# Kernel optimization log

Measured on AMD Instinct MI355X. Metric: run time of the kernel, lower is better.

Reference implementation:

```python
import jax, jax.numpy as jnp
import numpy as np

N = 100000   # nodes
E = 800000   # directed edges (symmetrized to 2E in forward)
D0 = 128     # input feature dim (dim0)
H = 128      # hidden = h_dim * args.d = 64 * 2
L = 4        # num_layers
G = 64       # num graphs for global_mean_pool
BN_EPS = 1e-5
LN_EPS = 1e-5


def setup_inputs() -> dict:
    key = jax.random.key(0)
    ks = jax.random.split(key, 12)
    s = 1.0 / np.sqrt(H)
    x = jax.random.normal(ks[0], (N, D0), dtype=jnp.float32)
    row = jax.random.randint(ks[1], (E,), 0, N, dtype=jnp.int32)
    off = jax.random.randint(ks[2], (E,), 1, N, dtype=jnp.int32)
    col = (row + off) % N  # guarantees row != col (no self loops)
    edge_index = jnp.stack([row, col])
    batch = jnp.sort(jax.random.randint(ks[3], (N,), 0, G, dtype=jnp.int32))
    return {
        "x": x,
        "W0": jax.random.normal(ks[4], (D0, H), dtype=jnp.float32) * s,
        "b0": jnp.zeros((H,), jnp.float32),
        "eps_l": jnp.zeros((L,), jnp.float32),        # GIN eps per layer
        "W1": jax.random.normal(ks[5], (L, H, H), dtype=jnp.float32) * s,
        "b1": jnp.zeros((L, H), jnp.float32),
        "bn_g": jnp.ones((L, H), jnp.float32),
        "bn_b": jnp.zeros((L, H), jnp.float32),
        "W2": jax.random.normal(ks[6], (L, H, H), dtype=jnp.float32) * s,
        "b2": jnp.zeros((L, H), jnp.float32),
        "ln_g": jnp.ones((L, H), jnp.float32),
        "ln_b": jnp.zeros((L, H), jnp.float32),
        "edge_index": edge_index,
        "batch": batch,
    }


def reference(x, W0, b0, eps_l, W1, b1, bn_g, bn_b, W2, b2, ln_g, ln_b, edge_index, batch):
    n = x.shape[0]
    h = x @ W0 + b0  # layer0 encode -> [N, H]
    # FNSD: symmetrize edges (cat with flip) and drop self loops
    ei = jnp.concatenate([edge_index, edge_index[::-1]], axis=1)
    row, col = ei[0], ei[1]
    w = (row != col).astype(h.dtype)  # self-loop removal as zero edge weight
    for i in range(L):
        # GINConv: scatter-add of neighbor features
        agg = jax.ops.segment_sum(w[:, None] * h[col], row, num_segments=n)
        u = (1.0 + eps_l[i]) * h + agg
        # mlp: Linear -> BatchNorm1d (training-mode batch stats) -> ReLU -> Linear
        z = u @ W1[i] + b1[i]
        m = jnp.mean(z, axis=0)
        v = jnp.var(z, axis=0)
        z = (z - m) * jax.lax.rsqrt(v + BN_EPS) * bn_g[i] + bn_b[i]
        z = jax.nn.relu(z)
        z = z @ W2[i] + b2[i]
        z = jax.nn.relu(z)          # use_activation
        h = h + z                    # use_residual
        mu = jnp.mean(h, axis=-1, keepdims=True)   # LayerNorm
        var = jnp.var(h, axis=-1, keepdims=True)
        h = (h - mu) * jax.lax.rsqrt(var + LN_EPS) * ln_g[i] + ln_b[i]
    # global_mean_pool over graph ids
    cnt = jax.ops.segment_sum(jnp.ones((n,), h.dtype), batch, num_segments=G)
    sums = jax.ops.segment_sum(h, batch, num_segments=G)
    return sums / jnp.maximum(cnt, 1.0)[:, None]
```

## Files before the change

kernel.cpp:

```cpp
#include <hip/hip_runtime.h>

#define NN 100000
#define EE 800000
#define HH 128
#define LL 4
#define GG 64
#define BN_EPS 1e-5f
#define LN_EPS 1e-5f
#define POOL_CHUNK 64
#define NBUK ((NN + 255) >> 8)
#define CAP 8192
#define BCHUNK 8192
#define UPITCH 136

typedef __attribute__((ext_vector_type(8))) short short8;
typedef __attribute__((ext_vector_type(4))) float f32x4;

__device__ inline unsigned short bf16_rne(float f) {
    unsigned u = __float_as_uint(f);
    return (unsigned short)((u + 0x7FFF + ((u >> 16) & 1)) >> 16);
}
__device__ inline float bf16_to_f32(unsigned short h) {
    return __uint_as_float((unsigned)h << 16);
}


__global__ void setup_kernel(const float* __restrict__ W0, const float* __restrict__ W1,
                             const float* __restrict__ W2, short* __restrict__ wt_hi,
                             int* __restrict__ bcur, float* __restrict__ colsum,
                             float* __restrict__ psum, float* __restrict__ pcnt) {
    int i = blockIdx.x * 256 + threadIdx.x;
    if (i < NBUK) bcur[i] = i * CAP;
    if (i < LL * HH * 2) colsum[i] = 0.f;
    if (i < GG * HH) psum[i] = 0.f;
    if (i < GG) pcnt[i] = 0.f;
    if (i < 9 * HH * HH) {
        int mat = i >> 14, rem = i & 16383;
        int n = rem >> 7, k = rem & 127;
        const float* src = (mat == 0) ? W0 : ((mat <= 4) ? W1 + (size_t)(mat - 1) * HH * HH
                                                         : W2 + (size_t)(mat - 5) * HH * HH);
        float v = src[(size_t)k * HH + n];
        int off = (mat << 14) + (((k >> 3) * 8 + (n >> 4)) << 7) + ((n & 15) << 3) + (k & 7);
        wt_hi[off] = (short)bf16_rne(v);
    }
}


__global__ __launch_bounds__(256) void bucket_scatter(const int* __restrict__ ei, int* __restrict__ bcur,
                                                      int* __restrict__ pairs) {
    __shared__ int h[NBUK];
    __shared__ int curb[NBUK];
    int tid = threadIdx.x;
    for (int i = tid; i < NBUK; i += 256) h[i] = 0;
    __syncthreads();
    int base = blockIdx.x * BCHUNK;
#pragma unroll 4
    for (int k = 0; k < BCHUNK / 256; k++) {
        int e = base + k * 256 + tid;
        if (e < 2 * EE) {
            int r = ei[e];
            int c = (e < EE) ? ei[e + EE] : ei[e - EE];
            if (r != c) atomicAdd(&h[r >> 8], 1);
        }
    }
    __syncthreads();
    for (int i = tid; i < NBUK; i += 256) {
        int n = h[i];
        curb[i] = n ? atomicAdd(&bcur[i], n) : 0;
    }
    __syncthreads();
#pragma unroll 4
    for (int k = 0; k < BCHUNK / 256; k++) {
        int e = base + k * 256 + tid;
        if (e < 2 * EE) {
            int r = ei[e];
            int c = (e < EE) ? ei[e + EE] : ei[e - EE];
            if (r != c) {
                int p = atomicAdd(&curb[r >> 8], 1);
                pairs[p] = ((r & 255) << 17) | c;
            }
        }
    }
}

__global__ __launch_bounds__(256) void bucket_build(const int* __restrict__ pairs, const int* __restrict__ bcur,
                                                    int* __restrict__ rp, int* __restrict__ re,
                                                    int* __restrict__ colidx) {
    __shared__ int hist[256], off[256], lcol[CAP];
    int b = blockIdx.x, tid = threadIdx.x;
    int s = b * CAP;
    int size = bcur[b] - s;
    hist[tid] = 0;
    __syncthreads();
    for (int i = tid; i < size; i += 256) atomicAdd(&hist[pairs[s + i] >> 17], 1);
    __syncthreads();
    off[tid] = hist[tid];
    __syncthreads();
    for (int o = 1; o < 256; o <<= 1) {
        int x = (tid >= o) ? off[tid - o] : 0;
        __syncthreads();
        off[tid] += x;
        __syncthreads();
    }
    int excl = (tid > 0) ? off[tid - 1] : 0;
    int r = (b << 8) + tid;
    if (r < NN) { rp[r] = s + excl; re[r] = s + off[tid]; }
    hist[tid] = excl;
    __syncthreads();
    for (int i = tid; i < size; i += 256) {
        int u = pairs[s + i];
        int p = atomicAdd(&hist[u >> 17], 1);
        lcol[p] = u & 0x1FFFF;
    }
    __syncthreads();
    for (int i = tid; i < size; i += 256) colidx[s + i] = lcol[i];
}


__global__ __launch_bounds__(256, 6) void fused_g1(
    const uint2* __restrict__ hbf2,
    const int* __restrict__ rp, const int* __restrict__ re,
    const int* __restrict__ colidx,
    const float* __restrict__ eps_l, int layer,
    const short* __restrict__ wt,
    const float* __restrict__ bias,
    unsigned short* __restrict__ z1_out,
    float* __restrict__ colsum, float* __restrict__ colsq)
{
    __shared__ __align__(16) unsigned short uls[64 * UPITCH];
    __shared__ float stats[2 * HH];
    int tid = threadIdx.x;
    int wave = tid >> 6, lane = tid & 63;
    int half = lane >> 5, sub = lane & 31;
    int lrow = lane & 15, kgrp = lane >> 4;
    int r0 = blockIdx.x * 64;
    stats[tid] = 0.f;
    float eps1 = 1.0f + eps_l[layer];

    int hw = wave * 2 + half;
    for (int rl = 0; rl < 8; rl++) {
        int row = hw * 8 + rl;
        int r = r0 + row;
        float a0 = 0.f, a1 = 0.f, a2 = 0.f, a3 = 0.f;
        if (r < NN) {
            uint2 sv = hbf2[(size_t)r * 32 + sub];
            a0 = bf16_to_f32((unsigned short)(sv.x & 0xFFFF)) * eps1;
            a1 = bf16_to_f32((unsigned short)(sv.x >> 16)) * eps1;
            a2 = bf16_to_f32((unsigned short)(sv.y & 0xFFFF)) * eps1;
            a3 = bf16_to_f32((unsigned short)(sv.y >> 16)) * eps1;
            int base = rp[r];
            int n = re[r] - base;
            for (int i = 0; i < n; i += 8) {
                uint2 v[8];
                int c[8];
#pragma unroll
                for (int j = 0; j < 8; j++) c[j] = (i + j < n) ? colidx[base + i + j] : -1;
#pragma unroll
                for (int j = 0; j < 8; j++)
                    v[j] = (c[j] >= 0) ? hbf2[(size_t)c[j] * 32 + sub] : make_uint2(0u, 0u);
#pragma unroll
                for (int j = 0; j < 8; j++) {
                    a0 += bf16_to_f32((unsigned short)(v[j].x & 0xFFFF));
                    a1 += bf16_to_f32((unsigned short)(v[j].x >> 16));
                    a2 += bf16_to_f32((unsigned short)(v[j].y & 0xFFFF));
                    a3 += bf16_to_f32((unsigned short)(v[j].y >> 16));
                }
            }
        }
        uint2 o;
        o.x = (unsigned)bf16_rne(a0) | ((unsigned)bf16_rne(a1) << 16);
        o.y = (unsigned)bf16_rne(a2) | ((unsigned)bf16_rne(a3) << 16);
        *(uint2*)&uls[row * UPITCH + sub * 4] = o;
    }
    __syncthreads();

    short8 az[4];
#pragma unroll
    for (int ks = 0; ks < 4; ks++)
        az[ks] = *(const short8*)&uls[(wave * 16 + lrow) * UPITCH + ks * 32 + kgrp * 8];
    __syncthreads();

    f32x4 acc[8];
#pragma unroll
    for (int c = 0; c < 8; c++) acc[c] = (f32x4){0.f, 0.f, 0.f, 0.f};
#pragma unroll
    for (int ks = 0; ks < 4; ks++) {
        int fb = (ks * 4 + kgrp) * 8;
#pragma unroll
        for (int c = 0; c < 8; c++) {
            short8 whi = *(const short8*)(wt + (size_t)((fb + c) << 7) + (lrow << 3));
            acc[c] = __builtin_amdgcn_mfma_f32_16x16x32_bf16(az[ks], whi, acc[c], 0, 0, 0);
        }
    }

    float bv[8];
#pragma unroll
    for (int c = 0; c < 8; c++) bv[c] = bias[c * 16 + lrow];
    int lrb = wave * 16 + kgrp * 4;
    float ps[8], pq[8];
#pragma unroll
    for (int c = 0; c < 8; c++) { ps[c] = 0.f; pq[c] = 0.f; }
#pragma unroll
    for (int c = 0; c < 8; c++)
#pragma unroll
        for (int reg = 0; reg < 4; reg++) {
            float z = acc[c][reg] + bv[c];
            uls[(lrb + reg) * UPITCH + c * 16 + lrow] = bf16_rne(z);
            if (r0 + lrb + reg < NN) { ps[c] += z; pq[c] += z * z; }
        }
#pragma unroll
    for (int c = 0; c < 8; c++) {
        ps[c] += __shfl_xor(ps[c], 16); pq[c] += __shfl_xor(pq[c], 16);
        ps[c] += __shfl_xor(ps[c], 32); pq[c] += __shfl_xor(pq[c], 32);
    }
    if (kgrp == 0) {
#pragma unroll
        for (int c = 0; c < 8; c++) {
            atomicAdd(&stats[c * 16 + lrow], ps[c]);
            atomicAdd(&stats[HH + c * 16 + lrow], pq[c]);
        }
    }
    __syncthreads();
#pragma unroll
    for (int i = 0; i < 4; i++) {
        int idx = tid + i * 256;
        int row = idx >> 4;
        int r = r0 + row;
        if (r < NN)
            *(uint4*)(z1_out + (size_t)r * HH + (idx & 15) * 8) =
                *(const uint4*)&uls[row * UPITCH + (idx & 15) * 8];
    }
    if (tid < HH) {
        atomicAdd(&colsum[tid], stats[tid]);
        atomicAdd(&colsq[tid], stats[HH + tid]);
    }
}


template<int MODE>
__global__ __launch_bounds__(256, 4) void gemm_v9(
    const void* __restrict__ Ain,
    const short* __restrict__ wt_hi,
    const float* __restrict__ bias,
    float* __restrict__ colsum, float* __restrict__ colsq,
    const float* __restrict__ bng, const float* __restrict__ bnb,
    const float* __restrict__ lng, const float* __restrict__ lnb,
    unsigned short* __restrict__ hbf)
{
    __shared__ short wh[HH * HH];
    __shared__ float stats[2 * HH];
    int tid = threadIdx.x;
    int wave = tid >> 6, lane = tid & 63;
    int lrow = lane & 15, kgrp = lane >> 4;
    int r0 = blockIdx.x * 64;
    int arow = r0 + wave * 16 + lrow;

    {
        const short8* src = (const short8*)wt_hi;
        short8* dst = (short8*)wh;
#pragma unroll
        for (int i = 0; i < 8; i++) dst[tid + i * 256] = src[tid + i * 256];
    }
    if (MODE == 2 && tid < HH) {
        float m = colsum[tid] * (1.f / NN);
        float v = colsq[tid] * (1.f / NN) - m * m;
        float a = bng[tid] * rsqrtf(v + BN_EPS);
        stats[tid] = a;
        stats[HH + tid] = bnb[tid] - m * a;
    }

    float4 a0[4], a1[4];
    short8 az[4];
    if (MODE == 2) {
        const unsigned short* Az = (const unsigned short*)Ain;
        if (arow < NN) {
#pragma unroll
            for (int ks = 0; ks < 4; ks++)
                az[ks] = *(const short8*)(Az + (size_t)arow * HH + ks * 32 + kgrp * 8);
        } else {
#pragma unroll
            for (int ks = 0; ks < 4; ks++) az[ks] = (short8){0,0,0,0,0,0,0,0};
        }
    } else {
        const float* Af = (const float*)Ain;
        if (arow < NN) {
#pragma unroll
            for (int ks = 0; ks < 4; ks++) {
                int kb = ks * 32 + kgrp * 8;
                a0[ks] = *(const float4*)(Af + (size_t)arow * HH + kb);
                a1[ks] = *(const float4*)(Af + (size_t)arow * HH + kb + 4);
            }
        } else {
#pragma unroll
            for (int ks = 0; ks < 4; ks++) {
                a0[ks] = make_float4(0.f, 0.f, 0.f, 0.f);
                a1[ks] = a0[ks];
            }
        }
    }
    __syncthreads();

    f32x4 acc[8];
#pragma unroll
    for (int c = 0; c < 8; c++) acc[c] = (f32x4){0.f, 0.f, 0.f, 0.f};

#pragma unroll
    for (int ks = 0; ks < 4; ks++) {
        int fb = (ks * 4 + kgrp) * 8;
        int kb = ks * 32 + kgrp * 8;
        float av[8];
        if (MODE == 2) {
#pragma unroll
            for (int j = 0; j < 8; j++) {
                float zb = bf16_to_f32((unsigned short)az[ks][j]);
                av[j] = fmaxf(fmaf(zb, stats[kb + j], stats[HH + kb + j]), 0.f);
            }
        } else {
            av[0] = a0[ks].x; av[1] = a0[ks].y; av[2] = a0[ks].z; av[3] = a0[ks].w;
            av[4] = a1[ks].x; av[5] = a1[ks].y; av[6] = a1[ks].z; av[7] = a1[ks].w;
        }
        short8 ahi, alo;
#pragma unroll
        for (int j = 0; j < 8; j++) {
            unsigned short hb = bf16_rne(av[j]);
            ahi[j] = (short)hb;
            alo[j] = (short)bf16_rne(av[j] - bf16_to_f32(hb));
        }
#pragma unroll
        for (int c = 0; c < 8; c++) {
            short8 whi = *(const short8*)(wh + ((fb + c) << 7) + (lrow << 3));
            acc[c] = __builtin_amdgcn_mfma_f32_16x16x32_bf16(ahi, whi, acc[c], 0, 0, 0);
            acc[c] = __builtin_amdgcn_mfma_f32_16x16x32_bf16(alo, whi, acc[c], 0, 0, 0);
        }
    }

    float bv[8];
#pragma unroll
    for (int c = 0; c < 8; c++) bv[c] = bias[c * 16 + lrow];
    int lrb = wave * 16 + kgrp * 4;
    unsigned short* hst = (unsigned short*)wh;

    if (MODE == 0) {
        __syncthreads();
#pragma unroll
        for (int c = 0; c < 8; c++)
#pragma unroll
            for (int reg = 0; reg < 4; reg++)
                hst[(lrb + reg) * HH + c * 16 + lrow] = bf16_rne(acc[c][reg] + bv[c]);
        __syncthreads();
#pragma unroll
        for (int i = 0; i < 4; i++) {
            int idx = tid + i * 256;
            int r = r0 + (idx >> 4);
            if (r < NN)
                *(uint4*)(hbf + (size_t)r * HH + (idx & 15) * 8) = ((const uint4*)wh)[idx];
        }
    } else {
        float lg[8], lb[8];
#pragma unroll
        for (int c = 0; c < 8; c++) {
            lg[c] = lng[c * 16 + lrow];
            lb[c] = lnb[c * 16 + lrow];
        }
        __syncthreads();
#pragma unroll
        for (int i = 0; i < 4; i++) {
            int idx = tid + i * 256;
            int r = r0 + (idx >> 4);
            uint4 v = make_uint4(0, 0, 0, 0);
            if (r < NN) v = *(const uint4*)(hbf + (size_t)r * HH + (idx & 15) * 8);
            ((uint4*)wh)[idx] = v;
        }
        __syncthreads();
#pragma unroll
        for (int reg = 0; reg < 4; reg++) {
            int r = r0 + lrb + reg;
            if (r < NN) {
                float tv[8];
                float s = 0.f, q = 0.f;
#pragma unroll
                for (int c = 0; c < 8; c++) {
                    float hold = bf16_to_f32(hst[(lrb + reg) * HH + c * 16 + lrow]);
                    tv[c] = hold + fmaxf(acc[c][reg] + bv[c], 0.f);
                    s += tv[c]; q += tv[c] * tv[c];
                }
#pragma unroll
                for (int m = 1; m < 16; m <<= 1) {
                    s += __shfl_xor(s, m);
                    q += __shfl_xor(q, m);
                }
                float mu = s * (1.f / 128.f);
                float var = q * (1.f / 128.f) - mu * mu;
                float rs = rsqrtf(var + LN_EPS);
#pragma unroll
                for (int c = 0; c < 8; c++)
                    hst[(lrb + reg) * HH + c * 16 + lrow] =
                        bf16_rne((tv[c] - mu) * rs * lg[c] + lb[c]);
            }
        }
        __syncthreads();
#pragma unroll
        for (int i = 0; i < 4; i++) {
            int idx = tid + i * 256;
            int r = r0 + (idx >> 4);
            if (r < NN)
                *(uint4*)(hbf + (size_t)r * HH + (idx & 15) * 8) = ((const uint4*)wh)[idx];
        }
    }
}


__global__ void pool_kernel(const unsigned short* __restrict__ h, const int* __restrict__ batch,
                            float* __restrict__ psum, float* __restrict__ pcnt)
{
    int t = threadIdx.x;
    int n0 = blockIdx.x * POOL_CHUNK;
    int n1 = n0 + POOL_CHUNK; if (n1 > NN) n1 = NN;
    if (n0 >= NN) return;
    float acc = 0.f;
    int cur = batch[n0];
    int cnt = 0;
    for (int n = n0; n < n1; n++) {
        int g = batch[n];
        if (g != cur) {
            atomicAdd(&psum[cur * HH + t], acc);
            if (t == 0) atomicAdd(&pcnt[cur], (float)cnt);
            acc = 0.f; cnt = 0; cur = g;
        }
        acc += bf16_to_f32(h[(size_t)n * HH + t]);
        cnt++;
    }
    atomicAdd(&psum[cur * HH + t], acc);
    if (t == 0) atomicAdd(&pcnt[cur], (float)cnt);
}

__global__ void pool_final(const float* __restrict__ psum, const float* __restrict__ pcnt,
                           float* __restrict__ out)
{
    int i = blockIdx.x * blockDim.x + threadIdx.x;
    if (i < GG * HH) {
        float c = pcnt[i >> 7];
        out[i] = psum[i] / fmaxf(c, 1.f);
    }
}


extern "C" void kernel_launch(void* const* d_in, const int* in_sizes, int n_in,
                              void* d_out, int out_size, void* d_ws, size_t ws_size,
                              hipStream_t stream)
{
    const float* x     = (const float*)d_in[0];
    const float* W0    = (const float*)d_in[1];
    const float* b0    = (const float*)d_in[2];
    const float* eps_l = (const float*)d_in[3];
    const float* W1    = (const float*)d_in[4];
    const float* b1    = (const float*)d_in[5];
    const float* bng   = (const float*)d_in[6];
    const float* bnb   = (const float*)d_in[7];
    const float* W2    = (const float*)d_in[8];
    const float* b2    = (const float*)d_in[9];
    const float* lng   = (const float*)d_in[10];
    const float* lnb   = (const float*)d_in[11];
    const int*   ei    = (const int*)d_in[12];
    const int*   batch = (const int*)d_in[13];
    float* out = (float*)d_out;

    char* ws = (char*)d_ws;
    size_t off = 0;
    auto alloc = [&](size_t bytes) -> void* {
        void* p = ws + off;
        off += (bytes + 255) & ~(size_t)255;
        return p;
    };
    unsigned short* hbf = (unsigned short*)alloc((size_t)NN * HH * 2);
    unsigned short* z1  = (unsigned short*)alloc((size_t)NN * HH * 2);
    int*   colidx = (int*)alloc((size_t)NBUK * CAP * 4 + 1024);
    int*   pairs  = (int*)alloc((size_t)NBUK * CAP * 4);
    int*   rp     = (int*)alloc((size_t)NN * 4);
    int*   re     = (int*)alloc((size_t)NN * 4);
    int*   bcur   = (int*)alloc((NBUK + 1) * 4);
    float* colsum = (float*)alloc((size_t)LL * HH * 2 * 4);
    float* psum   = (float*)alloc((size_t)GG * HH * 4);
    float* pcnt   = (float*)alloc(GG * 4);
    short* wt_hi  = (short*)alloc((size_t)9 * HH * HH * 2);

    setup_kernel<<<(9 * HH * HH + 255) / 256, 256, 0, stream>>>(W0, W1, W2, wt_hi, bcur,
                                                                colsum, psum, pcnt);

    bucket_scatter<<<(2 * EE + BCHUNK - 1) / BCHUNK, 256, 0, stream>>>(ei, bcur, pairs);
    bucket_build<<<NBUK, 256, 0, stream>>>(pairs, bcur, rp, re, colidx);

    int gb = (NN + 63) / 64;
    gemm_v9<0><<<gb, 256, 0, stream>>>(x, wt_hi, b0,
                                       nullptr, nullptr, nullptr, nullptr, nullptr, nullptr, hbf);

    for (int l = 0; l < LL; l++) {
        float* cs = colsum + (size_t)l * HH * 2;
        float* cq = cs + HH;
        fused_g1<<<gb, 256, 0, stream>>>((const uint2*)hbf, rp, re, colidx, eps_l, l,
                                         wt_hi + (size_t)(1 + l) * HH * HH, b1 + l * HH, z1,
                                         cs, cq);
        gemm_v9<2><<<gb, 256, 0, stream>>>(z1, wt_hi + (size_t)(5 + l) * HH * HH,
                                           b2 + l * HH,
                                           cs, cq, bng + l * HH, bnb + l * HH,
                                           lng + l * HH, lnb + l * HH, hbf);
    }

    pool_kernel<<<(NN + POOL_CHUNK - 1) / POOL_CHUNK, 128, 0, stream>>>(hbf, batch, psum, pcnt);
    pool_final<<<(GG * HH + 255) / 256, 256, 0, stream>>>(psum, pcnt, out);
}
```

Baseline: 675.0 us.

## Restructure GIN aggregation to 16-lane uint4 gathers with 32-row blocks

```diff
diff --git a/kernel.cpp b/kernel.cpp
--- a/kernel.cpp
+++ b/kernel.cpp
@@ -12,6 +12,7 @@
 #define CAP 8192
 #define BCHUNK 8192
 #define UPITCH 136
+#define BR 32
 
 typedef __attribute__((ext_vector_type(8))) short short8;
 typedef __attribute__((ext_vector_type(4))) float f32x4;
@@ -117,8 +118,8 @@
 }
 
 
-__global__ __launch_bounds__(256, 6) void fused_g1(
-    const uint2* __restrict__ hbf2,
+__global__ __launch_bounds__(256, 8) void fused_g1(
+    const uint4* __restrict__ hbf4,
     const int* __restrict__ rp, const int* __restrict__ re,
     const int* __restrict__ colidx,
     const float* __restrict__ eps_l, int layer,
@@ -127,102 +128,126 @@
     unsigned short* __restrict__ z1_out,
     float* __restrict__ colsum, float* __restrict__ colsq)
 {
-    __shared__ __align__(16) unsigned short uls[64 * UPITCH];
+    __shared__ __align__(16) unsigned short uls[BR * UPITCH];
     __shared__ float stats[2 * HH];
     int tid = threadIdx.x;
     int wave = tid >> 6, lane = tid & 63;
-    int half = lane >> 5, sub = lane & 31;
     int lrow = lane & 15, kgrp = lane >> 4;
-    int r0 = blockIdx.x * 64;
+    int sub = lrow;
+    int qw = wave * 4 + kgrp;
+    int r0 = blockIdx.x * BR;
     stats[tid] = 0.f;
     float eps1 = 1.0f + eps_l[layer];
 
-    int hw = wave * 2 + half;
-    for (int rl = 0; rl < 8; rl++) {
-        int row = hw * 8 + rl;
+    int base_[2], n_[2];
+#pragma unroll
+    for (int rl = 0; rl < 2; rl++) {
+        int r = r0 + qw * 2 + rl;
+        if (r < NN) { base_[rl] = rp[r]; n_[rl] = re[r] - base_[rl]; }
+        else        { base_[rl] = 0;     n_[rl] = 0; }
+    }
+    for (int rl = 0; rl < 2; rl++) {
+        int row = qw * 2 + rl;
         int r = r0 + row;
-        float a0 = 0.f, a1 = 0.f, a2 = 0.f, a3 = 0.f;
-        if (r < NN) {
-            uint2 sv = hbf2[(size_t)r * 32 + sub];
-            a0 = bf16_to_f32((unsigned short)(sv.x & 0xFFFF)) * eps1;
-            a1 = bf16_to_f32((unsigned short)(sv.x >> 16)) * eps1;
-            a2 = bf16_to_f32((unsigned short)(sv.y & 0xFFFF)) * eps1;
-            a3 = bf16_to_f32((unsigned short)(sv.y >> 16)) * eps1;
-            int base = rp[r];
-            int n = re[r] - base;
-            for (int i = 0; i < n; i += 8) {
-                uint2 v[8];
-                int c[8];
-#pragma unroll
-                for (int j = 0; j < 8; j++) c[j] = (i + j < n) ? colidx[base + i + j] : -1;
-#pragma unroll
-                for (int j = 0; j < 8; j++)
-                    v[j] = (c[j] >= 0) ? hbf2[(size_t)c[j] * 32 + sub] : make_uint2(0u, 0u);
-#pragma unroll
-                for (int j = 0; j < 8; j++) {
-                    a0 += bf16_to_f32((unsigned short)(v[j].x & 0xFFFF));
-                    a1 += bf16_to_f32((unsigned short)(v[j].x >> 16));
-                    a2 += bf16_to_f32((unsigned short)(v[j].y & 0xFFFF));
-                    a3 += bf16_to_f32((unsigned short)(v[j].y >> 16));
-                }
+        uint4 sv = make_uint4(0u, 0u, 0u, 0u);
+        if (r < NN) sv = hbf4[(size_t)r * 16 + sub];
+        int base = base_[rl], n = n_[rl];
+        float a[8];
+#pragma unroll
+        for (int j = 0; j < 8; j++) a[j] = 0.f;
+        for (int i = 0; i < n; i += 8) {
+            uint4 v[8];
+            int c[4];
+#pragma unroll
+            for (int j = 0; j < 4; j++) c[j] = (i + j < n) ? colidx[base + i + j] : -1;
+#pragma unroll
+            for (int j = 0; j < 4; j++)
+                v[j] = (c[j] >= 0) ? hbf4[(size_t)c[j] * 16 + sub] : make_uint4(0u, 0u, 0u, 0u);
+#pragma unroll
+            for (int j = 0; j < 4; j++) c[j] = (i + 4 + j < n) ? colidx[base + i + 4 + j] : -1;
+#pragma unroll
+            for (int j = 0; j < 4; j++)
+                v[4 + j] = (c[j] >= 0) ? hbf4[(size_t)c[j] * 16 + sub] : make_uint4(0u, 0u, 0u, 0u);
+#pragma unroll
+            for (int j = 0; j < 8; j++) {
+                a[0] += bf16_to_f32((unsigned short)(v[j].x & 0xFFFF));
+                a[1] += bf16_to_f32((unsigned short)(v[j].x >> 16));
+                a[2] += bf16_to_f32((unsigned short)(v[j].y & 0xFFFF));
+                a[3] += bf16_to_f32((unsigned short)(v[j].y >> 16));
+                a[4] += bf16_to_f32((unsigned short)(v[j].z & 0xFFFF));
+                a[5] += bf16_to_f32((unsigned short)(v[j].z >> 16));
+                a[6] += bf16_to_f32((unsigned short)(v[j].w & 0xFFFF));
+                a[7] += bf16_to_f32((unsigned short)(v[j].w >> 16));
             }
         }
-        uint2 o;
-        o.x = (unsigned)bf16_rne(a0) | ((unsigned)bf16_rne(a1) << 16);
-        o.y = (unsigned)bf16_rne(a2) | ((unsigned)bf16_rne(a3) << 16);
-        *(uint2*)&uls[row * UPITCH + sub * 4] = o;
-    }
-    __syncthreads();
-
+        a[0] += bf16_to_f32((unsigned short)(sv.x & 0xFFFF)) * eps1;
+        a[1] += bf16_to_f32((unsigned short)(sv.x >> 16)) * eps1;
+        a[2] += bf16_to_f32((unsigned short)(sv.y & 0xFFFF)) * eps1;
+        a[3] += bf16_to_f32((unsigned short)(sv.y >> 16)) * eps1;
+        a[4] += bf16_to_f32((unsigned short)(sv.z & 0xFFFF)) * eps1;
+        a[5] += bf16_to_f32((unsigned short)(sv.z >> 16)) * eps1;
+        a[6] += bf16_to_f32((unsigned short)(sv.w & 0xFFFF)) * eps1;
+        a[7] += bf16_to_f32((unsigned short)(sv.w >> 16)) * eps1;
+        uint4 o;
+        o.x = (unsigned)bf16_rne(a[0]) | ((unsigned)bf16_rne(a[1]) << 16);
+        o.y = (unsigned)bf16_rne(a[2]) | ((unsigned)bf16_rne(a[3]) << 16);
+        o.z = (unsigned)bf16_rne(a[4]) | ((unsigned)bf16_rne(a[5]) << 16);
+        o.w = (unsigned)bf16_rne(a[6]) | ((unsigned)bf16_rne(a[7]) << 16);
+        *(uint4*)&uls[row * UPITCH + sub * 8] = o;
+    }
+    __syncthreads();
+
+    int rowg = (wave & 1) * 16;
+    int colg = (wave >> 1) * 4;
     short8 az[4];
 #pragma unroll
     for (int ks = 0; ks < 4; ks++)
-        az[ks] = *(const short8*)&uls[(wave * 16 + lrow) * UPITCH + ks * 32 + kgrp * 8];
-    __syncthreads();
-
-    f32x4 acc[8];
-#pragma unroll
-    for (int c = 0; c < 8; c++) acc[c] = (f32x4){0.f, 0.f, 0.f, 0.f};
+        az[ks] = *(const short8*)&uls[(rowg + lrow) * UPITCH + ks * 32 + kgrp * 8];
+    __syncthreads();
+
+    f32x4 acc[4];
+#pragma unroll
+    for (int c = 0; c < 4; c++) acc[c] = (f32x4){0.f, 0.f, 0.f, 0.f};
 #pragma unroll
     for (int ks = 0; ks < 4; ks++) {
         int fb = (ks * 4 + kgrp) * 8;
 #pragma unroll
-        for (int c = 0; c < 8; c++) {
-            short8 whi = *(const short8*)(wt + (size_t)((fb + c) << 7) + (lrow << 3));
+        for (int c = 0; c < 4; c++) {
+            short8 whi = *(const short8*)(wt + (size_t)((fb + colg + c) << 7) + (lrow << 3));
             acc[c] = __builtin_amdgcn_mfma_f32_16x16x32_bf16(az[ks], whi, acc[c], 0, 0, 0);
         }
     }
 
-    float bv[8];
-#pragma unroll
-    for (int c = 0; c < 8; c++) bv[c] = bias[c * 16 + lrow];
-    int lrb = wave * 16 + kgrp * 4;
-    float ps[8], pq[8];
-#pragma unroll
-    for (int c = 0; c < 8; c++) { ps[c] = 0.f; pq[c] = 0.f; }
-#pragma unroll
-    for (int c = 0; c < 8; c++)
+    float bv[4];
+#pragma unroll
+    for (int c = 0; c < 4; c++) bv[c] = bias[(colg + c) * 16 + lrow];
+    int lrb = rowg + kgrp * 4;
+    float ps[4], pq[4];
+#pragma unroll
+    for (int c = 0; c < 4; c++) { ps[c] = 0.f; pq[c] = 0.f; }
+#pragma unroll
+    for (int c = 0; c < 4; c++)
 #pragma unroll
         for (int reg = 0; reg < 4; reg++) {
             float z = acc[c][reg] + bv[c];
-            uls[(lrb + reg) * UPITCH + c * 16 + lrow] = bf16_rne(z);
+            uls[(lrb + reg) * UPITCH + (colg + c) * 16 + lrow] = bf16_rne(z);
             if (r0 + lrb + reg < NN) { ps[c] += z; pq[c] += z * z; }
         }
 #pragma unroll
-    for (int c = 0; c < 8; c++) {
+    for (int c = 0; c < 4; c++) {
         ps[c] += __shfl_xor(ps[c], 16); pq[c] += __shfl_xor(pq[c], 16);
         ps[c] += __shfl_xor(ps[c], 32); pq[c] += __shfl_xor(pq[c], 32);
     }
     if (kgrp == 0) {
 #pragma unroll
-        for (int c = 0; c < 8; c++) {
-            atomicAdd(&stats[c * 16 + lrow], ps[c]);
-            atomicAdd(&stats[HH + c * 16 + lrow], pq[c]);
-        }
-    }
-    __syncthreads();
-#pragma unroll
-    for (int i = 0; i < 4; i++) {
+        for (int c = 0; c < 4; c++) {
+            atomicAdd(&stats[(colg + c) * 16 + lrow], ps[c]);
+            atomicAdd(&stats[HH + (colg + c) * 16 + lrow], pq[c]);
+        }
+    }
+    __syncthreads();
+#pragma unroll
+    for (int i = 0; i < 2; i++) {
         int idx = tid + i * 256;
         int row = idx >> 4;
         int r = r0 + row;
@@ -491,15 +516,16 @@
     bucket_build<<<NBUK, 256, 0, stream>>>(pairs, bcur, rp, re, colidx);
 
     int gb = (NN + 63) / 64;
+    int gb1 = (NN + BR - 1) / BR;
     gemm_v9<0><<<gb, 256, 0, stream>>>(x, wt_hi, b0,
                                        nullptr, nullptr, nullptr, nullptr, nullptr, nullptr, hbf);
 
     for (int l = 0; l < LL; l++) {
         float* cs = colsum + (size_t)l * HH * 2;
         float* cq = cs + HH;
-        fused_g1<<<gb, 256, 0, stream>>>((const uint2*)hbf, rp, re, colidx, eps_l, l,
-                                         wt_hi + (size_t)(1 + l) * HH * HH, b1 + l * HH, z1,
-                                         cs, cq);
+        fused_g1<<<gb1, 256, 0, stream>>>((const uint4*)hbf, rp, re, colidx, eps_l, l,
+                                          wt_hi + (size_t)(1 + l) * HH * HH, b1 + l * HH, z1,
+                                          cs, cq);
         gemm_v9<2><<<gb, 256, 0, stream>>>(z1, wt_hi + (size_t)(5 + l) * HH * HH,
                                            b2 + l * HH,
                                            cs, cq, bng + l * HH, bnb + l * HH,
```

After: 1.020 ms. 1.51x slower.
